# Performance work log

Measured on AMD Instinct MI355X. Metric: run time of the kernel, lower is better.

## Reference

```python
import jax, jax.numpy as jnp
import numpy as np

N = 512          # number of proposals
C = 1024         # in_channels
FLAT = C * 7 * 7 # 50176, fc1 input dim
D = 1024         # hidden / feat_dim / attention dim
SCALE = 1.0 / np.sqrt(float(D))


def setup_inputs() -> dict:
    key = jax.random.key(0)
    ks = jax.random.split(key, 20)
    w = lambda k, shape: (jax.random.normal(k, shape, jnp.float32) * 0.01)
    inp = {"x": jax.random.normal(ks[0], (N, C, 7, 7), jnp.float32)}
    # SelsaHead fc layers
    inp["fc1_w"] = w(ks[1], (D, FLAT)); inp["fc1_b"] = jnp.zeros((D,), jnp.float32)
    inp["fc2_w"] = w(ks[2], (D, D));    inp["fc2_b"] = jnp.zeros((D,), jnp.float32)
    # attention_1 (semantic_aggregation): fc1, fc2, 1x1 conv (stored as [D,D] matrix)
    inp["a1_fc1_w"] = w(ks[3], (D, D)); inp["a1_fc1_b"] = jnp.zeros((D,), jnp.float32)
    inp["a1_fc2_w"] = w(ks[4], (D, D)); inp["a1_fc2_b"] = jnp.zeros((D,), jnp.float32)
    inp["a1_conv_w"] = w(ks[5], (D, D)); inp["a1_conv_b"] = jnp.zeros((D,), jnp.float32)
    # attention_2
    inp["a2_fc1_w"] = w(ks[6], (D, D)); inp["a2_fc1_b"] = jnp.zeros((D,), jnp.float32)
    inp["a2_fc2_w"] = w(ks[7], (D, D)); inp["a2_fc2_b"] = jnp.zeros((D,), jnp.float32)
    inp["a2_conv_w"] = w(ks[8], (D, D)); inp["a2_conv_b"] = jnp.zeros((D,), jnp.float32)
    return inp


def _semantic_aggregation(x, w1, b1, w2, b2, cw, cb):
    # x: [N, D]. Single-head dense attention over proposals, values = x itself.
    q = x @ w1.T + b1                      # [N, D]
    k = x @ w2.T + b2                      # [N, D]
    p = jax.nn.softmax((q @ k.T) * SCALE, axis=-1)  # [N, N]
    out = p @ x                            # [N, D]  (values are raw x)
    return out @ cw.T + cb                 # 1x1 conv == linear [N, D]


def reference(x, fc1_w, fc1_b, fc2_w, fc2_b,
              a1_fc1_w, a1_fc1_b, a1_fc2_w, a1_fc2_b, a1_conv_w, a1_conv_b,
              a2_fc1_w, a2_fc1_b, a2_fc2_w, a2_fc2_b, a2_conv_w, a2_conv_b):
    out = x.reshape(x.shape[0], -1) @ fc1_w.T + fc1_b        # [N, D]
    r1 = _semantic_aggregation(out, a1_fc1_w, a1_fc1_b, a1_fc2_w, a1_fc2_b,
                               a1_conv_w, a1_conv_b)
    h = jax.nn.relu(out + r1)
    h = h @ fc2_w.T + fc2_b                                  # [N, D]
    r2 = _semantic_aggregation(h, a2_fc1_w, a2_fc1_b, a2_fc2_w, a2_fc2_b,
                               a2_conv_w, a2_conv_b)
    return jax.nn.relu(h + r2 + out)                         # [N, D]
```

## Files before the change

kernel.cpp:

```cpp
#include <hip/hip_runtime.h>
#include <hip/hip_bf16.h>

typedef __attribute__((ext_vector_type(8))) short short8;
typedef __attribute__((ext_vector_type(4))) float f32x4;

#define N_PROP 512
#define DHID   1024
#define KFLAT  50176
#define SM_SCALE 0.03125f

__device__ inline short f2bf(float x) {
  __hip_bfloat16 b = __float2bfloat16(x);
  return __builtin_bit_cast(short, b);
}
__device__ inline float bf2f(unsigned short u) {
  unsigned int x = (unsigned int)u << 16;
  return __builtin_bit_cast(float, x);
}

__device__ inline void pinned_bar() {
  asm volatile("s_waitcnt lgkmcnt(0)" ::: "memory");
  __builtin_amdgcn_s_barrier();
  asm volatile("" ::: "memory");
}

__global__ __launch_bounds__(1024, 4)
void gemm_fc1(const float* __restrict__ A, const float* __restrict__ B,
              __hip_bfloat16* __restrict__ parts)
{
  constexpr int BK = 32;
  constexpr int KLEN = 1568, NT = KLEN / BK;
  __shared__ short sA[2][256 * 32];
  __shared__ short sB[2][256 * 32];

  const int n = gridDim.x;
  int lid = blockIdx.x;
  lid = (lid & 7) * (n >> 3) + (lid >> 3);
  const int y    = lid >> 3;
  const int tile = lid & 7;
  const int tm = tile >> 2;
  const int tn = tile & 3;

  const int k0 = y * KLEN;

  const int tid  = threadIdx.x;
  const int lane = tid & 63;
  const int wid  = tid >> 6;
  const int wr = wid >> 2, wc = wid & 3;
  const int l16 = lane & 15, kq = lane >> 4;

  const float* Ab = A + (size_t)(tm * 256) * KFLAT;
  const float* Bb = B + (size_t)(tn * 256) * KFLAT;

  const int srow = tid >> 2;
  const int sc   = tid & 3;
  const int sphys = sc ^ ((srow >> 1) & 3);

  f32x4 acc[4][4];
  #pragma unroll
  for (int i = 0; i < 4; ++i)
    #pragma unroll
    for (int j = 0; j < 4; ++j)
      acc[i][j] = (f32x4){0.f, 0.f, 0.f, 0.f};

  float4 ra0, ra1;
  f32x4  rb0, rb1;

  auto loadAB = [&](int kk) {
    const float* pa = Ab + (size_t)srow * KFLAT + kk + sc * 8;
    const float* pb = Bb + (size_t)srow * KFLAT + kk + sc * 8;
    ra0 = *(const float4*)pa; ra1 = *(const float4*)(pa + 4);
    rb0 = __builtin_nontemporal_load((const f32x4*)pb);
    rb1 = __builtin_nontemporal_load((const f32x4*)pb + 1);
  };
  auto storeAB = [&](int b) {
    short8 s;
    s[0]=f2bf(ra0.x); s[1]=f2bf(ra0.y); s[2]=f2bf(ra0.z); s[3]=f2bf(ra0.w);
    s[4]=f2bf(ra1.x); s[5]=f2bf(ra1.y); s[6]=f2bf(ra1.z); s[7]=f2bf(ra1.w);
    *(short8*)&sA[b][srow * 32 + sphys * 8] = s;
    s[0]=f2bf(rb0[0]); s[1]=f2bf(rb0[1]); s[2]=f2bf(rb0[2]); s[3]=f2bf(rb0[3]);
    s[4]=f2bf(rb1[0]); s[5]=f2bf(rb1[1]); s[6]=f2bf(rb1[2]); s[7]=f2bf(rb1[3]);
    *(short8*)&sB[b][srow * 32 + sphys * 8] = s;
  };
  auto compute = [&](int b) {
    short8 af[4], bf[4];
    #pragma unroll
    for (int i = 0; i < 4; ++i) {
      int R  = wr * 64 + i * 16 + l16;
      int ph = kq ^ ((R >> 1) & 3);
      af[i] = *(short8*)&sA[b][R * 32 + ph * 8];
    }
    #pragma unroll
    for (int j = 0; j < 4; ++j) {
      int R  = wc * 64 + j * 16 + l16;
      int ph = kq ^ ((R >> 1) & 3);
      bf[j] = *(short8*)&sB[b][R * 32 + ph * 8];
    }
    #pragma unroll
    for (int i = 0; i < 4; ++i)
      #pragma unroll
      for (int j = 0; j < 4; ++j)
        acc[i][j] = __builtin_amdgcn_mfma_f32_16x16x32_bf16(af[i], bf[j], acc[i][j], 0, 0, 0);
  };

  loadAB(k0);
  storeAB(0);
  loadAB(k0 + BK);
  pinned_bar();

  int cur = 0;
  for (int t = 0; t < NT; ++t) {
    if (t + 1 < NT) {
      storeAB(cur ^ 1);
      if (t + 2 < NT) loadAB(k0 + (t + 2) * BK);
    }
    compute(cur);
    pinned_bar();
    cur ^= 1;
  }

  __hip_bfloat16* P = parts + (size_t)y * (N_PROP * DHID);
  const int crow0 = tm * 256 + wr * 64;
  const int ccol0 = tn * 256 + wc * 64;
  #pragma unroll
  for (int i = 0; i < 4; ++i)
    #pragma unroll
    for (int j = 0; j < 4; ++j)
      #pragma unroll
      for (int e = 0; e < 4; ++e) {
        int r = crow0 + i * 16 + kq * 4 + e;
        int c = ccol0 + j * 16 + l16;
        P[(size_t)r * DHID + c] = __float2bfloat16(acc[i][j][e]);
      }
}

template<int BM, int BN, int BK, typename BT>
__global__ __launch_bounds__(256, 2)
void gemm_bf(const __hip_bfloat16* __restrict__ A, int lda,
             const BT* __restrict__ B1, const BT* __restrict__ B2,
             const BT* __restrict__ B3, int ldb,
             float* __restrict__ C, __hip_bfloat16* __restrict__ Cb, int ldc,
             int tiles_n, int ktot, size_t c_z_stride,
             const float* __restrict__ bias1, const float* __restrict__ bias2,
             const float* __restrict__ bias3,
             const float* __restrict__ res1, const float* __restrict__ res2,
             __hip_bfloat16* __restrict__ Ct, int ldct, int ct_z, int do_relu)
{
  constexpr int BKP = BK + 8;
  constexpr int WM = BM / 2, WN = BN / 2;
  constexpr int FM = WM / 16, FN = WN / 16;
  constexpr int NC = BK / 8;
  constexpr int NA = (BM * BK) / (8 * 256);
  constexpr int NB = (BN * BK) / (8 * 256);
  constexpr bool BF = sizeof(BT) == 2;

  __shared__ short As[2][BM * BKP];
  __shared__ short Bs[2][BN * BKP];

  const int n = gridDim.x;
  int lid = blockIdx.x;
  lid = (lid & 7) * (n >> 3) + (lid >> 3);
  const int tm = lid / tiles_n;
  const int tn = lid % tiles_n;
  const int nt = ktot / BK;

  if (C)  C  += (size_t)blockIdx.z * c_z_stride;
  if (Cb) Cb += (size_t)blockIdx.z * c_z_stride;
  const BT* B       = blockIdx.z == 0 ? B1 : (blockIdx.z == 1 ? B2 : B3);
  const float* bias = blockIdx.z == 0 ? bias1 : (blockIdx.z == 1 ? bias2 : bias3);
  const bool wr_ct  = Ct && ((int)blockIdx.z == ct_z);

  const int tid  = threadIdx.x;
  const int lane = tid & 63;
  const int wid  = tid >> 6;
  const int wm = wid >> 1, wn = wid & 1;
  const int l16 = lane & 15, kq = lane >> 4;

  const __hip_bfloat16* Ab = A + (size_t)(tm * BM) * lda;
  const BT*             Bb = B + (size_t)(tn * BN) * ldb;

  f32x4 acc[FM][FN];
  #pragma unroll
  for (int i = 0; i < FM; ++i)
    #pragma unroll
    for (int j = 0; j < FN; ++j)
      acc[i][j] = (f32x4){0.f, 0.f, 0.f, 0.f};

  short8 a0[NA]; short8 b0h[NB]; float4 b0f[NB][2];
  short8 a1[NA]; short8 b1h[NB]; float4 b1f[NB][2];

  auto load0 = [&](int kk) {
    #pragma unroll
    for (int i = 0; i < NA; ++i) {
      int ch = tid + i * 256; int r = ch / NC, c = (ch % NC) * 8;
      a0[i] = *(const short8*)(Ab + (size_t)r * lda + kk + c);
    }
    #pragma unroll
    for (int i = 0; i < NB; ++i) {
      int ch = tid + i * 256; int r = ch / NC, c = (ch % NC) * 8;
      if constexpr (BF) b0h[i] = *(const short8*)(Bb + (size_t)r * ldb + kk + c);
      else {
        const float* p = (const float*)Bb + (size_t)r * ldb + kk + c;
        b0f[i][0] = *(const float4*)p; b0f[i][1] = *(const float4*)(p + 4);
      }
    }
  };
  auto load1 = [&](int kk) {
    #pragma unroll
    for (int i = 0; i < NA; ++i) {
      int ch = tid + i * 256; int r = ch / NC, c = (ch % NC) * 8;
      a1[i] = *(const short8*)(Ab + (size_t)r * lda + kk + c);
    }
    #pragma unroll
    for (int i = 0; i < NB; ++i) {
      int ch = tid + i * 256; int r = ch / NC, c = (ch % NC) * 8;
      if constexpr (BF) b1h[i] = *(const short8*)(Bb + (size_t)r * ldb + kk + c);
      else {
        const float* p = (const float*)Bb + (size_t)r * ldb + kk + c;
        b1f[i][0] = *(const float4*)p; b1f[i][1] = *(const float4*)(p + 4);
      }
    }
  };
  auto store0 = [&](int buf) {
    #pragma unroll
    for (int i = 0; i < NA; ++i) {
      int ch = tid + i * 256; int r = ch / NC, c = (ch % NC) * 8;
      *(short8*)&As[buf][r * BKP + c] = a0[i];
    }
    #pragma unroll
    for (int i = 0; i < NB; ++i) {
      int ch = tid + i * 256; int r = ch / NC, c = (ch % NC) * 8;
      if constexpr (BF) *(short8*)&Bs[buf][r * BKP + c] = b0h[i];
      else {
        float4 u = b0f[i][0], v = b0f[i][1];
        short8 w;
        w[0]=f2bf(u.x); w[1]=f2bf(u.y); w[2]=f2bf(u.z); w[3]=f2bf(u.w);
        w[4]=f2bf(v.x); w[5]=f2bf(v.y); w[6]=f2bf(v.z); w[7]=f2bf(v.w);
        *(short8*)&Bs[buf][r * BKP + c] = w;
      }
    }
  };
  auto store1 = [&](int buf) {
    #pragma unroll
    for (int i = 0; i < NA; ++i) {
      int ch = tid + i * 256; int r = ch / NC, c = (ch % NC) * 8;
      *(short8*)&As[buf][r * BKP + c] = a1[i];
    }
    #pragma unroll
    for (int i = 0; i < NB; ++i) {
      int ch = tid + i * 256; int r = ch / NC, c = (ch % NC) * 8;
      if constexpr (BF) *(short8*)&Bs[buf][r * BKP + c] = b1h[i];
      else {
        float4 u = b1f[i][0], v = b1f[i][1];
        short8 w;
        w[0]=f2bf(u.x); w[1]=f2bf(u.y); w[2]=f2bf(u.z); w[3]=f2bf(u.w);
        w[4]=f2bf(v.x); w[5]=f2bf(v.y); w[6]=f2bf(v.z); w[7]=f2bf(v.w);
        *(short8*)&Bs[buf][r * BKP + c] = w;
      }
    }
  };
  auto compute = [&](int buf) {
    #pragma unroll
    for (int ks = 0; ks < BK / 32; ++ks) {
      short8 af[FM], bf[FN];
      #pragma unroll
      for (int i = 0; i < FM; ++i)
        af[i] = *(short8*)&As[buf][(wm * WM + i * 16 + l16) * BKP + ks * 32 + kq * 8];
      #pragma unroll
      for (int j = 0; j < FN; ++j)
        bf[j] = *(short8*)&Bs[buf][(wn * WN + j * 16 + l16) * BKP + ks * 32 + kq * 8];
      #pragma unroll
      for (int i = 0; i < FM; ++i)
        #pragma unroll
        for (int j = 0; j < FN; ++j)
          acc[i][j] = __builtin_amdgcn_mfma_f32_16x16x32_bf16(af[i], bf[j], acc[i][j], 0, 0, 0);
    }
  };

  load0(0);
  store0(0);
  load1(BK);
  pinned_bar();

  int t = 0;
  for (; t + 2 < nt; t += 2) {
    store1(1); load0((t + 2) * BK);
    compute(0); pinned_bar();
    store0(0); load1((t + 3) * BK);
    compute(1); pinned_bar();
  }
  store1(1);
  compute(0); pinned_bar();
  compute(1);

  const int crow0 = tm * BM + wm * WM;
  const int ccol0 = tn * BN + wn * WN;
  #pragma unroll
  for (int i = 0; i < FM; ++i)
    #pragma unroll
    for (int j = 0; j < FN; ++j)
      #pragma unroll
      for (int e = 0; e < 4; ++e) {
        int r = crow0 + i * 16 + kq * 4 + e;
        int c = ccol0 + j * 16 + l16;
        float v = acc[i][j][e];
        if (bias) v += bias[c];
        if (res1) v += res1[(size_t)r * ldc + c];
        if (res2) v += res2[(size_t)r * ldc + c];
        if (do_relu) v = fmaxf(v, 0.f);
        if (C)  C [(size_t)r * ldc + c] = v;
        if (Cb) Cb[(size_t)r * ldc + c] = __float2bfloat16(v);
        if (wr_ct) Ct[(size_t)c * ldct + r] = __float2bfloat16(v);
      }
}

__global__ __launch_bounds__(256)
void reduce_s(const __hip_bfloat16* __restrict__ parts, const float* __restrict__ bias,
              float* __restrict__ out0f, __hip_bfloat16* __restrict__ out0b)
{
  int idx4 = blockIdx.x * 256 + threadIdx.x;
  int c4 = idx4 & (DHID / 4 - 1);
  float4 b = *(const float4*)(bias + (size_t)c4 * 4);
  float s0 = b.x, s1 = b.y, s2 = b.z, s3 = b.w;
  for (int i = 0; i < 32; ++i) {
    ushort4 u = *(const ushort4*)(parts + (size_t)i * (N_PROP * DHID) +
                                  (size_t)idx4 * 4);
    s0 += bf2f(u.x); s1 += bf2f(u.y); s2 += bf2f(u.z); s3 += bf2f(u.w);
  }
  float4 o = {s0, s1, s2, s3};
  *(float4*)(out0f + (size_t)idx4 * 4) = o;
  ushort4 ob = {(unsigned short)f2bf(s0), (unsigned short)f2bf(s1),
                (unsigned short)f2bf(s2), (unsigned short)f2bf(s3)};
  *(ushort4*)(out0b + (size_t)idx4 * 4) = ob;
}

__global__ __launch_bounds__(256)
void softmax_rows(const float* __restrict__ x, __hip_bfloat16* __restrict__ p, float scale)
{
  int row = blockIdx.x;
  const float* q = x + (size_t)row * N_PROP;
  int tid = threadIdx.x;
  float a = q[tid] * scale;
  float b = q[tid + 256] * scale;
  float m = fmaxf(a, b);
  #pragma unroll
  for (int o = 32; o > 0; o >>= 1) m = fmaxf(m, __shfl_xor(m, o));
  __shared__ float sm[4], ss[4];
  int w = tid >> 6;
  if ((tid & 63) == 0) sm[w] = m;
  __syncthreads();
  m = fmaxf(fmaxf(sm[0], sm[1]), fmaxf(sm[2], sm[3]));
  float ea = __expf(a - m), eb = __expf(b - m);
  float s = ea + eb;
  #pragma unroll
  for (int o = 32; o > 0; o >>= 1) s += __shfl_xor(s, o);
  if ((tid & 63) == 0) ss[w] = s;
  __syncthreads();
  s = ss[0] + ss[1] + ss[2] + ss[3];
  float inv = 1.f / s;
  p[(size_t)row * N_PROP + tid]       = __float2bfloat16(ea * inv);
  p[(size_t)row * N_PROP + tid + 256] = __float2bfloat16(eb * inv);
}

extern "C" void kernel_launch(void* const* d_in, const int* in_sizes, int n_in,
                              void* d_out, int out_size, void* d_ws, size_t ws_size,
                              hipStream_t stream)
{
  (void)in_sizes; (void)n_in; (void)out_size; (void)ws_size;
  const float* x      = (const float*)d_in[0];
  const float* fc1_w  = (const float*)d_in[1];
  const float* fc1_b  = (const float*)d_in[2];
  const float* fc2_w  = (const float*)d_in[3];
  const float* fc2_b  = (const float*)d_in[4];
  const float* a1w1   = (const float*)d_in[5];
  const float* a1b1   = (const float*)d_in[6];
  const float* a1w2   = (const float*)d_in[7];
  const float* a1b2   = (const float*)d_in[8];
  const float* a1cw   = (const float*)d_in[9];
  const float* a1cb   = (const float*)d_in[10];
  const float* a2w1   = (const float*)d_in[11];
  const float* a2b1   = (const float*)d_in[12];
  const float* a2w2   = (const float*)d_in[13];
  const float* a2b2   = (const float*)d_in[14];
  const float* a2cw   = (const float*)d_in[15];
  const float* a2cb   = (const float*)d_in[16];
  float* out = (float*)d_out;

  typedef __hip_bfloat16 bf16;
  char* ws = (char*)d_ws;
  const size_t MB = 1024 * 1024;
  float* out0f  = (float*)(ws + 0 * MB);
  float* h1f    = (float*)(ws + 2 * MB);
  float* logits = (float*)(ws + 4 * MB);
  bf16*  out0b  = (bf16*)(ws + 5 * MB);
  bf16*  h0b    = (bf16*)(ws + 6 * MB);
  bf16*  q      = (bf16*)(ws + 7 * MB);
  bf16*  k      = (bf16*)(ws + 8 * MB);
  bf16*  Vt     = (bf16*)(ws + 10 * MB);
  bf16*  h1b    = (bf16*)(ws + 11 * MB);
  bf16*  pb     = (bf16*)(ws + 12 * MB);
  bf16*  parts  = (bf16*)(ws + 13 * MB);
  const size_t ND = (size_t)N_PROP * DHID;
  dim3 blk(256);

  gemm_fc1<<<dim3(256), dim3(1024), 0, stream>>>(x, fc1_w, parts);
  reduce_s<<<dim3(512), blk, 0, stream>>>(parts, fc1_b, out0f, out0b);

  gemm_bf<32, 64, 128, float><<<dim3(256, 1, 3), blk, 0, stream>>>(
      out0b, DHID, a1w1, a1w2, a1cw, DHID,
      nullptr, q, DHID, 16, DHID, ND,
      a1b1, a1b2, a1cb, nullptr, nullptr, Vt, N_PROP, 2, 0);
  gemm_bf<32, 32, 128, bf16><<<dim3(256), blk, 0, stream>>>(
      q, DHID, k, nullptr, nullptr, DHID,
      logits, nullptr, N_PROP, 16, DHID, 0,
      nullptr, nullptr, nullptr, nullptr, nullptr, nullptr, 0, -1, 0);
  softmax_rows<<<N_PROP, blk, 0, stream>>>(logits, pb, SM_SCALE);
  gemm_bf<32, 64, 128, bf16><<<dim3(256), blk, 0, stream>>>(
      pb, N_PROP, Vt, nullptr, nullptr, N_PROP,
      nullptr, h0b, DHID, 16, N_PROP, 0,
      nullptr, nullptr, nullptr, out0f, nullptr, nullptr, 0, -1, 1);
  gemm_bf<32, 64, 128, float><<<dim3(256), blk, 0, stream>>>(
      h0b, DHID, fc2_w, nullptr, nullptr, DHID,
      h1f, h1b, DHID, 16, DHID, 0,
      fc2_b, nullptr, nullptr, nullptr, nullptr, nullptr, 0, -1, 0);

  gemm_bf<32, 64, 128, float><<<dim3(256, 1, 3), blk, 0, stream>>>(
      h1b, DHID, a2w1, a2w2, a2cw, DHID,
      nullptr, q, DHID, 16, DHID, ND,
      a2b1, a2b2, a2cb, nullptr, nullptr, Vt, N_PROP, 2, 0);
  gemm_bf<32, 32, 128, bf16><<<dim3(256), blk, 0, stream>>>(
      q, DHID, k, nullptr, nullptr, DHID,
      logits, nullptr, N_PROP, 16, DHID, 0,
      nullptr, nullptr, nullptr, nullptr, nullptr, nullptr, 0, -1, 0);
  softmax_rows<<<N_PROP, blk, 0, stream>>>(logits, pb, SM_SCALE);
  gemm_bf<32, 64, 128, bf16><<<dim3(256), blk, 0, stream>>>(
      pb, N_PROP, Vt, nullptr, nullptr, N_PROP,
      out, nullptr, DHID, 16, N_PROP, 0,
      nullptr, nullptr, nullptr, h1f, out0f, nullptr, 0, -1, 1);
}
```

Baseline: 185.5 us.

## Fuse QK^T logits GEMM with row softmax into one kernel

Replaces the separate Q·K^T GEMM (writing fp32 logits) and the row-wise softmax kernel with a single kernel. Each block computes 32 full rows of logits across all 512 keys in registers and applies a block-level max/sum reduction before writing bf16 probabilities. This removes one launch and the fp32 logits round trip through memory. The trade-off is that only 16 blocks are launched and each block streams the whole K matrix, so parallelism is much lower than in the 256-block GEMM.

Result: slower. 233.1 us (+25.6%).

```diff
diff --git a/kernel.cpp b/kernel.cpp
--- a/kernel.cpp
+++ b/kernel.cpp
@@ -314,6 +314,161 @@
       }
 }
 
+__global__ __launch_bounds__(256, 2)
+void qk_softmax(const __hip_bfloat16* __restrict__ Q,
+                const __hip_bfloat16* __restrict__ Km,
+                __hip_bfloat16* __restrict__ P)
+{
+  constexpr int BK = 32, BKP = 40, NTS = DHID / BK;
+  __shared__ short Asq[2][32 * BKP];
+  __shared__ short Bsk[2][512 * BKP];
+  __shared__ float redm[32][4];
+  __shared__ float reds[32][4];
+
+  const int r0  = blockIdx.x * 32;
+  const int tid = threadIdx.x;
+  const int lane = tid & 63;
+  const int w = tid >> 6;
+  const int l16 = lane & 15, kq = lane >> 4;
+
+  const __hip_bfloat16* Qb = Q + (size_t)r0 * DHID;
+
+  f32x4 acc[2][8];
+  #pragma unroll
+  for (int i = 0; i < 2; ++i)
+    #pragma unroll
+    for (int j = 0; j < 8; ++j)
+      acc[i][j] = (f32x4){0.f, 0.f, 0.f, 0.f};
+
+  short8 b0s[8], b1s[8]; short8 a0s, a1s;
+
+  auto load0 = [&](int kk) {
+    #pragma unroll
+    for (int i = 0; i < 8; ++i) {
+      int ch = tid + i * 256; int r = ch >> 2, c = (ch & 3) * 8;
+      b0s[i] = *(const short8*)(Km + (size_t)r * DHID + kk + c);
+    }
+    if (tid < 128) {
+      int r = tid >> 2, c = (tid & 3) * 8;
+      a0s = *(const short8*)(Qb + (size_t)r * DHID + kk + c);
+    }
+  };
+  auto load1 = [&](int kk) {
+    #pragma unroll
+    for (int i = 0; i < 8; ++i) {
+      int ch = tid + i * 256; int r = ch >> 2, c = (ch & 3) * 8;
+      b1s[i] = *(const short8*)(Km + (size_t)r * DHID + kk + c);
+    }
+    if (tid < 128) {
+      int r = tid >> 2, c = (tid & 3) * 8;
+      a1s = *(const short8*)(Qb + (size_t)r * DHID + kk + c);
+    }
+  };
+  auto store0 = [&](int buf) {
+    #pragma unroll
+    for (int i = 0; i < 8; ++i) {
+      int ch = tid + i * 256; int r = ch >> 2, c = (ch & 3) * 8;
+      *(short8*)&Bsk[buf][r * BKP + c] = b0s[i];
+    }
+    if (tid < 128) {
+      int r = tid >> 2, c = (tid & 3) * 8;
+      *(short8*)&Asq[buf][r * BKP + c] = a0s;
+    }
+  };
+  auto store1 = [&](int buf) {
+    #pragma unroll
+    for (int i = 0; i < 8; ++i) {
+      int ch = tid + i * 256; int r = ch >> 2, c = (ch & 3) * 8;
+      *(short8*)&Bsk[buf][r * BKP + c] = b1s[i];
+    }
+    if (tid < 128) {
+      int r = tid >> 2, c = (tid & 3) * 8;
+      *(short8*)&Asq[buf][r * BKP + c] = a1s;
+    }
+  };
+  auto compute = [&](int buf) {
+    short8 af[2], bf[8];
+    #pragma unroll
+    for (int i = 0; i < 2; ++i)
+      af[i] = *(short8*)&Asq[buf][(i * 16 + l16) * BKP + kq * 8];
+    #pragma unroll
+    for (int j = 0; j < 8; ++j)
+      bf[j] = *(short8*)&Bsk[buf][(w * 128 + j * 16 + l16) * BKP + kq * 8];
+    #pragma unroll
+    for (int i = 0; i < 2; ++i)
+      #pragma unroll
+      for (int j = 0; j < 8; ++j)
+        acc[i][j] = __builtin_amdgcn_mfma_f32_16x16x32_bf16(af[i], bf[j], acc[i][j], 0, 0, 0);
+  };
+
+  load0(0);
+  store0(0);
+  load1(BK);
+  pinned_bar();
+
+  int t = 0;
+  for (; t + 2 < NTS; t += 2) {
+    store1(1); load0((t + 2) * BK);
+    compute(0); pinned_bar();
+    store0(0); load1((t + 3) * BK);
+    compute(1); pinned_bar();
+  }
+  store1(1);
+  compute(0); pinned_bar();
+  compute(1);
+  __syncthreads();
+
+  float mx[2][4];
+  #pragma unroll
+  for (int i = 0; i < 2; ++i)
+    #pragma unroll
+    for (int e = 0; e < 4; ++e) {
+      float m = acc[i][0][e];
+      #pragma unroll
+      for (int j = 1; j < 8; ++j) m = fmaxf(m, acc[i][j][e]);
+      #pragma unroll
+      for (int o = 8; o > 0; o >>= 1) m = fmaxf(m, __shfl_xor(m, o));
+      mx[i][e] = m;
+      if (l16 == 0) redm[i * 16 + kq * 4 + e][w] = m;
+    }
+  __syncthreads();
+  float M[2][4], S[2][4];
+  #pragma unroll
+  for (int i = 0; i < 2; ++i)
+    #pragma unroll
+    for (int e = 0; e < 4; ++e) {
+      int r = i * 16 + kq * 4 + e;
+      float m = fmaxf(fmaxf(redm[r][0], redm[r][1]),
+                      fmaxf(redm[r][2], redm[r][3])) * SM_SCALE;
+      M[i][e] = m;
+      float s = 0.f;
+      #pragma unroll
+      for (int j = 0; j < 8; ++j) {
+        float p = __expf(acc[i][j][e] * SM_SCALE - m);
+        acc[i][j][e] = p;
+        s += p;
+      }
+      #pragma unroll
+      for (int o = 8; o > 0; o >>= 1) s += __shfl_xor(s, o);
+      if (l16 == 0) reds[r][w] = s;
+      S[i][e] = s;
+    }
+  __syncthreads();
+  #pragma unroll
+  for (int i = 0; i < 2; ++i)
+    #pragma unroll
+    for (int e = 0; e < 4; ++e) {
+      int r = i * 16 + kq * 4 + e;
+      float inv = 1.f / (reds[r][0] + reds[r][1] + reds[r][2] + reds[r][3]);
+      #pragma unroll
+      for (int j = 0; j < 8; ++j) {
+        int col = w * 128 + j * 16 + l16;
+        P[(size_t)(r0 + r) * N_PROP + col] = __float2bfloat16(acc[i][j][e] * inv);
+      }
+    }
+  (void)mx; (void)M; (void)S;
+}
+
 __global__ __launch_bounds__(256)
 void reduce_s(const __hip_bfloat16* __restrict__ parts, const float* __restrict__ bias,
               float* __restrict__ out0f, __hip_bfloat16* __restrict__ out0b)
@@ -332,34 +487,6 @@
   ushort4 ob = {(unsigned short)f2bf(s0), (unsigned short)f2bf(s1),
                 (unsigned short)f2bf(s2), (unsigned short)f2bf(s3)};
   *(ushort4*)(out0b + (size_t)idx4 * 4) = ob;
-}
-
-__global__ __launch_bounds__(256)
-void softmax_rows(const float* __restrict__ x, __hip_bfloat16* __restrict__ p, float scale)
-{
-  int row = blockIdx.x;
-  const float* q = x + (size_t)row * N_PROP;
-  int tid = threadIdx.x;
-  float a = q[tid] * scale;
-  float b = q[tid + 256] * scale;
-  float m = fmaxf(a, b);
-  #pragma unroll
-  for (int o = 32; o > 0; o >>= 1) m = fmaxf(m, __shfl_xor(m, o));
-  __shared__ float sm[4], ss[4];
-  int w = tid >> 6;
-  if ((tid & 63) == 0) sm[w] = m;
-  __syncthreads();
-  m = fmaxf(fmaxf(sm[0], sm[1]), fmaxf(sm[2], sm[3]));
-  float ea = __expf(a - m), eb = __expf(b - m);
-  float s = ea + eb;
-  #pragma unroll
-  for (int o = 32; o > 0; o >>= 1) s += __shfl_xor(s, o);
-  if ((tid & 63) == 0) ss[w] = s;
-  __syncthreads();
-  s = ss[0] + ss[1] + ss[2] + ss[3];
-  float inv = 1.f / s;
-  p[(size_t)row * N_PROP + tid]       = __float2bfloat16(ea * inv);
-  p[(size_t)row * N_PROP + tid + 256] = __float2bfloat16(eb * inv);
 }
 
 extern "C" void kernel_launch(void* const* d_in, const int* in_sizes, int n_in,
@@ -391,7 +518,6 @@
   const size_t MB = 1024 * 1024;
   float* out0f  = (float*)(ws + 0 * MB);
   float* h1f    = (float*)(ws + 2 * MB);
-  float* logits = (float*)(ws + 4 * MB);
   bf16*  out0b  = (bf16*)(ws + 5 * MB);
   bf16*  h0b    = (bf16*)(ws + 6 * MB);
   bf16*  q      = (bf16*)(ws + 7 * MB);
@@ -410,11 +536,7 @@
       out0b, DHID, a1w1, a1w2, a1cw, DHID,
       nullptr, q, DHID, 16, DHID, ND,
       a1b1, a1b2, a1cb, nullptr, nullptr, Vt, N_PROP, 2, 0);
-  gemm_bf<32, 32, 128, bf16><<<dim3(256), blk, 0, stream>>>(
-      q, DHID, k, nullptr, nullptr, DHID,
-      logits, nullptr, N_PROP, 16, DHID, 0,
-      nullptr, nullptr, nullptr, nullptr, nullptr, nullptr, 0, -1, 0);
-  softmax_rows<<<N_PROP, blk, 0, stream>>>(logits, pb, SM_SCALE);
+  qk_softmax<<<dim3(16), blk, 0, stream>>>(q, k, pb);
   gemm_bf<32, 64, 128, bf16><<<dim3(256), blk, 0, stream>>>(
       pb, N_PROP, Vt, nullptr, nullptr, N_PROP,
       nullptr, h0b, DHID, 16, N_PROP, 0,
@@ -428,11 +550,7 @@
       h1b, DHID, a2w1, a2w2, a2cw, DHID,
       nullptr, q, DHID, 16, DHID, ND,
       a2b1, a2b2, a2cb, nullptr, nullptr, Vt, N_PROP, 2, 0);
-  gemm_bf<32, 32, 128, bf16><<<dim3(256), blk, 0, stream>>>(
-      q, DHID, k, nullptr, nullptr, DHID,
-      logits, nullptr, N_PROP, 16, DHID, 0,
-      nullptr, nullptr, nullptr, nullptr, nullptr, nullptr, 0, -1, 0);
-  softmax_rows<<<N_PROP, blk, 0, stream>>>(logits, pb, SM_SCALE);
+  qk_softmax<<<dim3(16), blk, 0, stream>>>(q, k, pb);
   gemm_bf<32, 64, 128, bf16><<<dim3(256), blk, 0, stream>>>(
       pb, N_PROP, Vt, nullptr, nullptr, N_PROP,
       out, nullptr, DHID, 16, N_PROP, 0,
```
